# Kernel optimization log

Hardware: AMD Instinct MI355X
Metric: run time of the kernel (lower is better)

The kernel has to match this reference:

```python
import jax, jax.numpy as jnp
import numpy as np

N = 50000          # nodes
E = 400000         # edges (before self loops)
F_IN = 128         # NUM_FEATURES
HID = 32           # hidden_dim
H = 12             # heads
HC = H * HID       # concat dim = 384
CLASSES = 40       # NUM_CLASSES
NEG_SLOPE = 0.2    # PyG GATv2 default


def setup_inputs() -> dict:
    key = jax.random.key(0)
    ks = jax.random.split(key, 16)

    def p(k, shape, fan_in):
        return (jax.random.normal(k, shape, jnp.float32) / np.sqrt(fan_in)).astype(jnp.float32)

    return {
        "x": jax.random.normal(ks[0], (N, F_IN), jnp.float32),
        "edge_index": jax.random.randint(ks[1], (2, E), 0, N, jnp.int32),
        # GATv2 layer 1 (share_weights=False)
        "Wl1": p(ks[2], (F_IN, HC), F_IN),
        "Wr1": p(ks[3], (F_IN, HC), F_IN),
        "a1": p(ks[4], (H, HID), HID),
        "b1": jnp.zeros((HC,), jnp.float32),
        # GATv2 layer 2
        "Wl2": p(ks[5], (HC, HC), HC),
        "Wr2": p(ks[6], (HC, HC), HC),
        "a2": p(ks[7], (H, HID), HID),
        "b2": jnp.zeros((HC,), jnp.float32),
        # MLP head
        "W3": p(ks[8], (HC, HID), HC),
        "b3": jnp.zeros((HID,), jnp.float32),
        "W4": p(ks[9], (HID, CLASSES), HID),
        "b4": jnp.zeros((CLASSES,), jnp.float32),
    }


def _gatv2(x, Wl, Wr, att, bias, src, dst):
    # source/target linear projections, per-head
    xl = (x @ Wl).reshape(-1, H, HID)   # [N,H,C] (message features)
    xr = (x @ Wr).reshape(-1, H, HID)   # [N,H,C]
    # per-edge attention logits: a^T LeakyReLU(xl_src + xr_dst)
    e = jax.nn.leaky_relu(xl[src] + xr[dst], NEG_SLOPE)   # [E',H,C]
    logit = jnp.einsum('ehc,hc->eh', e, att)              # [E',H]
    # segment softmax over incoming edges per dst node (self loops guarantee nonempty)
    m = jax.ops.segment_max(logit, dst, num_segments=N)   # [N,H]
    ex = jnp.exp(logit - m[dst])
    denom = jax.ops.segment_sum(ex, dst, num_segments=N)  # [N,H]
    alpha = ex / denom[dst]                                # [E',H]
    # weighted scatter-add of source messages
    out = jax.ops.segment_sum(xl[src] * alpha[:, :, None], dst, num_segments=N)
    return out.reshape(-1, HC) + bias


def reference(x, edge_index, Wl1, Wr1, a1, b1, Wl2, Wr2, a2, b2, W3, b3, W4, b4):
    # add_self_loops=True (PyG default)
    loops = jnp.arange(N, dtype=edge_index.dtype)
    src = jnp.concatenate([edge_index[0], loops])
    dst = jnp.concatenate([edge_index[1], loops])
    # dropout p=0.6 is identity in eval mode
    h = _gatv2(x, Wl1, Wr1, a1, b1, src, dst)
    h = jax.nn.elu(h)
    h = _gatv2(h, Wl2, Wr2, a2, b2, src, dst)
    h = jax.nn.elu(h)
    h = jax.nn.elu(h @ W3 + b3)
    h = h @ W4 + b4
    return jax.nn.log_softmax(h, axis=1)
```

## Files before the change

kernel.cpp:

```cpp
#include <hip/hip_runtime.h>
#include <hip/hip_bf16.h>
#include <math.h>

#define N_NODES 50000
#define E_EDGES 400000
#define EN_TOT  (E_EDGES + N_NODES)
#define F_IN    128
#define HC      384
#define CLASSES 40
#define LOG2E   1.44269504088896f

typedef short short8 __attribute__((ext_vector_type(8)));
typedef float floatx4 __attribute__((ext_vector_type(4)));
typedef float floatx2 __attribute__((ext_vector_type(2)));
typedef unsigned int uint;

struct u3 { uint x, y, z; };

__device__ __forceinline__ float bf2f(unsigned short u) {
  union { unsigned int i; float f; } x; x.i = ((unsigned int)u) << 16; return x.f;
}
__device__ __forceinline__ unsigned short f2bf(float f) {
  union { float f; unsigned int i; } x; x.f = f;
  unsigned int r = x.i + 0x7fffu + ((x.i >> 16) & 1u);
  return (unsigned short)(r >> 16);
}
__device__ __forceinline__ float fin(float v) {
  return (fabsf(v) < 1e30f) ? v : 0.f;
}
__device__ __forceinline__ float rdw(const void* p, int idx, int fp32) {
  return fp32 ? ((const float*)p)[idx] : bf2f(((const unsigned short*)p)[idx]);
}

#if __has_builtin(__builtin_amdgcn_exp2f)
#define EXP2F(x) __builtin_amdgcn_exp2f(x)
#else
#define EXP2F(x) exp2f(x)
#endif

#if __has_builtin(__builtin_amdgcn_update_dpp)
#define DPP_ADD(w, ctrl) \
  (w += __int_as_float(__builtin_amdgcn_update_dpp(0, __float_as_int(w), ctrl, 0xf, 0xf, true)))
#define REDUCE16(w) do { DPP_ADD(w, 0xB1); DPP_ADD(w, 0x4E); DPP_ADD(w, 0x141); DPP_ADD(w, 0x140); } while (0)
#define DPP_MAXF(w, ctrl) do { float _t = __int_as_float(__builtin_amdgcn_update_dpp(0, \
    __float_as_int(w), ctrl, 0xf, 0xf, true)); w = fmaxf(w, _t); } while (0)
#define RED16MAX(w) do { DPP_MAXF(w, 0xB1); DPP_MAXF(w, 0x4E); DPP_MAXF(w, 0x141); DPP_MAXF(w, 0x140); } while (0)
#else
#define REDUCE16(w) do { w += __shfl_xor(w, 1); w += __shfl_xor(w, 2); \
                         w += __shfl_xor(w, 4); w += __shfl_xor(w, 8); } while (0)
#define RED16MAX(w) do { w = fmaxf(w, __shfl_xor(w, 1)); w = fmaxf(w, __shfl_xor(w, 2)); \
                         w = fmaxf(w, __shfl_xor(w, 4)); w = fmaxf(w, __shfl_xor(w, 8)); } while (0)
#endif


__global__ void k_sentinel(float* out, int n) {
  int i = blockIdx.x * 256 + threadIdx.x;
  if (i < n) out[i] = 111.0f;
}

__global__ void k_detect_zero(const unsigned short* __restrict__ x, int* __restrict__ flag,
                              int* __restrict__ counts, int* __restrict__ cursor) {
  int i = blockIdx.x * 256 + threadIdx.x;
  if (i < N_NODES) { counts[i] = 0; cursor[i] = 0; }
  if (blockIdx.x == 0 && threadIdx.x < 64) {
    int L = threadIdx.x;
    int sane = 0;
#pragma unroll
    for (int t = 0; t < 4; ++t) {
      unsigned short u = x[(size_t)(L * 4 + t) * 2];
      unsigned int mag = u & 0x7FFFu;
      unsigned int e   = (u >> 7) & 0xFFu;
      if (mag == 0u || (e >= 96u && e <= 159u)) sane++;
    }
    sane += __shfl_xor(sane, 1);
    sane += __shfl_xor(sane, 2);
    sane += __shfl_xor(sane, 4);
    sane += __shfl_xor(sane, 8);
    sane += __shfl_xor(sane, 16);
    sane += __shfl_xor(sane, 32);
    if (L == 0) flag[0] = (sane < 179) ? 1 : 0;
  }
}

__global__ void k_cvt(const void* __restrict__ x, unsigned short* __restrict__ Xb,
                      const int* __restrict__ flagp) {
  int i = blockIdx.x * 256 + threadIdx.x;
  if (i >= N_NODES * F_IN / 8) return;
  if (flagp[0]) {
    const floatx4* p = (const floatx4*)x + (size_t)i * 2;
    floatx4 f0 = p[0], f1 = p[1];
    short8 o;
#pragma unroll
    for (int j = 0; j < 4; ++j) { o[j] = (short)f2bf(f0[j]); o[4 + j] = (short)f2bf(f1[j]); }
    ((short8*)Xb)[i] = o;
  } else {
    ((short8*)Xb)[i] = ((const short8*)x)[i];
  }
}

__global__ void k_count(const int* __restrict__ ei, int* __restrict__ counts) {
  int e = blockIdx.x * 256 + threadIdx.x;
  if (e >= EN_TOT) return;
  int dst = (e < E_EDGES) ? ei[E_EDGES + e] : (e - E_EDGES);
  if ((unsigned)dst < N_NODES) atomicAdd(&counts[dst], 1);
}

__global__ void k_scan1(const int* __restrict__ counts, int* __restrict__ row_start,
                        int* __restrict__ bsum) {
  int b = blockIdx.x, tid = threadIdx.x;
  int i = b * 1024 + tid;
  int v = (i < N_NODES) ? counts[i] : 0;
  int lane = tid & 63, w = tid >> 6;
  int x = v;
#pragma unroll
  for (int d = 1; d < 64; d <<= 1) { int t = __shfl_up(x, d); if (lane >= d) x += t; }
  __shared__ int wsum[16];
  if (lane == 63) wsum[w] = x;
  __syncthreads();
  if (w == 0) {
    int y = (lane < 16) ? wsum[lane] : 0;
#pragma unroll
    for (int d = 1; d < 16; d <<= 1) { int t = __shfl_up(y, d); if (lane >= d) y += t; }
    if (lane < 16) wsum[lane] = y;
  }
  __syncthreads();
  if (w > 0) x += wsum[w - 1];
  if (i < N_NODES) row_start[i + 1] = x;
  if (tid == 1023) bsum[b] = x;
}

__global__ void k_scan23(int* __restrict__ row_start, const int* __restrict__ bsum, int nb) {
  int b = blockIdx.x, tid = threadIdx.x;
  __shared__ int sadd;
  if (tid < 64) {
    int lane = tid;
    int x = (lane < nb) ? bsum[lane] : 0;
#pragma unroll
    for (int d = 1; d < 64; d <<= 1) { int t = __shfl_up(x, d); if (lane >= d) x += t; }
    int pre = __shfl(x, (b > 0) ? (b - 1) : 0);
    if (tid == 0) sadd = (b > 0) ? pre : 0;
  }
  __syncthreads();
  int add = sadd;
  int i = b * 1024 + tid;
  if (i < N_NODES) row_start[i + 1] += add;
  if (i == 0) row_start[0] = 0;
}

__global__ void k_fill(const int* __restrict__ ei, const int* __restrict__ row_start,
                       int* __restrict__ cursor, int* __restrict__ csr_off) {
  int e = blockIdx.x * 256 + threadIdx.x;
  if (e >= EN_TOT) return;
  int src, dst;
  if (e < E_EDGES) { src = ei[e]; dst = ei[E_EDGES + e]; }
  else             { src = dst = e - E_EDGES; }
  if ((unsigned)dst >= N_NODES) return;
  int sv = ((unsigned)src < N_NODES) ? src : 0;
  int pos = atomicAdd(&cursor[dst], 1);
  int slot = row_start[dst] + pos;
  if ((unsigned)slot < EN_TOT) csr_off[slot] = sv * 768;
}

#define PK_J1 (F_IN * HC)
#define PK_J2 (2 * PK_J1)
#define PK_J3 (PK_J2 + HC * HC)
#define PK_J4 (PK_J3 + HC * HC)
#define PK_J5 (PK_J4 + HC * 32)
#define PK_J6 (PK_J5 + 32 * 48)
#define PK_EX 3144
#define PK_TOT (PK_J6 + PK_EX)
__global__ void k_pack_all(const void* __restrict__ Wl1, const void* __restrict__ Wr1,
                           const void* __restrict__ Wl2, const void* __restrict__ Wr2,
                           const void* __restrict__ W3, const void* __restrict__ W4,
                           const void* __restrict__ a1_, const void* __restrict__ a2_,
                           const void* __restrict__ b1_, const void* __restrict__ b2_,
                           const void* __restrict__ b3_, const void* __restrict__ b4_,
                           unsigned short* __restrict__ BpL1, unsigned short* __restrict__ BpR1,
                           unsigned short* __restrict__ BpL2, unsigned short* __restrict__ BpR2,
                           unsigned short* __restrict__ Bp3, unsigned short* __restrict__ Bp4,
                           float* __restrict__ attp1, float* __restrict__ attp2,
                           float* __restrict__ biasp1, float* __restrict__ biasp2,
                           float* __restrict__ b3p, float* __restrict__ b4p,
                           const int* __restrict__ flagp) {
  int gid = blockIdx.x * 256 + threadIdx.x;
  if (gid >= PK_TOT) return;
  int fp32 = flagp[0];
  if (gid >= PK_J6) {
    int i = gid - PK_J6;
    if (i < 3072) {
      int seg = i / 768, r = i % 768;
      int L = r / 6, q = r % 6, k = q >> 1, b = q & 1;
      int c = 2 * L + 128 * k + b;
      if (seg == 0)      attp1[r]  = fin(rdw(a1_, c, fp32)) * LOG2E;
      else if (seg == 1) attp2[r]  = fin(rdw(a2_, c, fp32)) * LOG2E;
      else if (seg == 2) biasp1[r] = fin(rdw(b1_, c, fp32));
      else               biasp2[r] = fin(rdw(b2_, c, fp32));
    } else if (i < 3104) b3p[i - 3072] = fin(rdw(b3_, i - 3072, fp32));
    else                 b4p[i - 3104] = fin(rdw(b4_, i - 3104, fp32));
    return;
  }
  const void* src; unsigned short* dst; int NT, NCOL, idx;
  if (gid < PK_J2)      { NT = 24; NCOL = 384; if (gid < PK_J1) { src = Wl1; dst = BpL1; idx = gid; }
                                               else             { src = Wr1; dst = BpR1; idx = gid - PK_J1; } }
  else if (gid < PK_J4) { NT = 24; NCOL = 384; if (gid < PK_J3) { src = Wl2; dst = BpL2; idx = gid - PK_J2; }
                                               else             { src = Wr2; dst = BpR2; idx = gid - PK_J3; } }
  else if (gid < PK_J5) { NT = 2;  NCOL = 32;  src = W3; dst = Bp3; idx = gid - PK_J4; }
  else                  { NT = 3;  NCOL = 40;  src = W4; dst = Bp4; idx = gid - PK_J5; }
  int j  = idx & 7;
  int L  = (idx >> 3) & 63;
  int t  = idx >> 9;
  int nt = t % NT;
  int kt = t / NT;
  int k  = kt * 32 + ((L >> 4) * 8) + j;
  int n  = nt * 16 + (L & 15);
  float v = (n < NCOL) ? rdw(src, k * NCOL + n, fp32) : 0.f;
  dst[idx] = f2bf(fin(v));
}

#define LOADB(dst, kt) do { _Pragma("unroll") for (int n = 0; n < 6; ++n) \
    dst[n] = ((const short8*)Bp)[((size_t)((kt) * 24 + nt0 + n)) * 64 + lane]; } while (0)
#define DOMFMA(bf, kt) do { \
    short8 af[2]; \
    _Pragma("unroll") for (int mf = 0; mf < 2; ++mf) { \
      int row = mf * 16 + rsel; \
      int col = (kt) * 64 + kk16 * 16; \
      af[mf] = *(const short8*)(smem + row * RS + (col ^ ((row & 7) << 4))); } \
    _Pragma("unroll") for (int n = 0; n < 6; ++n) \
      _Pragma("unroll") for (int mf = 0; mf < 2; ++mf) \
        acc[mf][n] = __builtin_amdgcn_mfma_f32_16x16x32_bf16(af[mf], bf[n], acc[mf][n], 0, 0, 0); } while (0)

template<int NK>
__global__ __launch_bounds__(256, 4) void k_gemm2(const unsigned short* __restrict__ A_,
                       const unsigned short* __restrict__ BpL,
                       const unsigned short* __restrict__ BpR,
                       unsigned short* __restrict__ CL, unsigned short* __restrict__ CR) {
  constexpr int RS  = NK * 64;
  constexpr int NST = NK / 2;
  __shared__ __align__(16) char smem[32 * 776];
  int which = blockIdx.x & 1;
  int bt    = blockIdx.x >> 1;
  const unsigned short* Bp = which ? BpR : BpL;
  unsigned short* C        = which ? CR  : CL;
  int tid  = threadIdx.x;
  int wave = tid >> 6, lane = tid & 63;
  int m0   = bt * 32;

  {
    uint4 v[NST];
#pragma unroll
    for (int i = 0; i < NST; ++i) {
      int o   = (i * 256 + tid) * 16;
      int row = o / RS;
      int rem = o - row * RS;
      int rg  = m0 + row; if (rg >= N_NODES) rg = N_NODES - 1;
      v[i] = *(const uint4*)((const char*)A_ + (size_t)rg * RS + rem);
    }
#pragma unroll
    for (int i = 0; i < NST; ++i) {
      int o   = (i * 256 + tid) * 16;
      int row = o / RS;
      int rem = o - row * RS;
      *(uint4*)(smem + row * RS + (rem ^ ((row & 7) << 4))) = v[i];
    }
  }

  int nt0  = wave * 6;
  int kk16 = (lane >> 4);
  int rsel = lane & 15;
  floatx4 acc[2][6];
#pragma unroll
  for (int mf = 0; mf < 2; ++mf)
#pragma unroll
    for (int n = 0; n < 6; ++n) acc[mf][n] = (floatx4){0.f, 0.f, 0.f, 0.f};

  short8 b0[6], b1[6], b2[6];
  LOADB(b0, 0);
  LOADB(b1, 1);
  __syncthreads();

#pragma unroll
  for (int kt = 0; kt < NK; ++kt) {
    if (kt + 2 < NK) {
      if (((kt + 2) % 3) == 0)      LOADB(b0, kt + 2);
      else if (((kt + 2) % 3) == 1) LOADB(b1, kt + 2);
      else                          LOADB(b2, kt + 2);
    }
    if ((kt % 3) == 0)      DOMFMA(b0, kt);
    else if ((kt % 3) == 1) DOMFMA(b1, kt);
    else                    DOMFMA(b2, kt);
  }

  __syncthreads();
  int qr = lane >> 4, ccol = lane & 15;
#pragma unroll
  for (int n = 0; n < 6; ++n) {
    int c    = (nt0 + n) * 16 + ccol;
    int soff = ((c & 127) >> 1) * 12 + (c >> 7) * 4 + (c & 1) * 2;
#pragma unroll
    for (int mf = 0; mf < 2; ++mf)
#pragma unroll
      for (int r = 0; r < 4; ++r) {
        int row = mf * 16 + qr * 4 + r;
        *(unsigned short*)(smem + row * 776 + soff) = f2bf(fin(acc[mf][n][r]));
      }
  }
  __syncthreads();
#pragma unroll
  for (int j = 0; j < 8; ++j) {
    int row = wave * 8 + j;
    int rg  = m0 + row;
    if (rg < N_NODES) {
      u3 val = *(const u3*)(smem + row * 776 + lane * 12);
      *(u3*)((char*)C + (size_t)rg * 768 + lane * 12) = val;
    }
  }
}

#define EBODY(q) do { \
    uint _qa[3] = {(q).x, (q).y, (q).z}; \
    _Pragma("unroll") \
    for (int k = 0; k < 3; ++k) { \
      floatx2 sv; \
      sv.x = __uint_as_float(_qa[k] << 16); \
      sv.y = __uint_as_float(_qa[k] & 0xffff0000u); \
      floatx2 t = sv + r2[k]; \
      t = __builtin_elementwise_max(t, t * 0.2f); \
      floatx2 dw = t * a2[k]; \
      float w = dw.x + dw.y; \
      REDUCE16(w); \
      w = fminf(fmaxf(w, -126.f), 126.f); \
      float p = EXP2F(w); \
      l[k] += p; \
      floatx2 pv = {p, p}; \
      acc[k] += pv * sv; \
    } } while (0)

__global__ void k_edge(const unsigned short* __restrict__ XL, const unsigned short* __restrict__ XR,
                       const int* __restrict__ row_start, const int* __restrict__ csr_off,
                       const float* __restrict__ attp, const float* __restrict__ biasp,
                       unsigned short* __restrict__ H) {
  int v = blockIdx.x;
  int L = threadIdx.x;
  int Lo = L * 12;
  floatx2 r2[3], a2[3];
  u3 rv3 = *(const u3*)((const char*)XR + (size_t)v * 768 + Lo);
  uint rr[3] = {rv3.x, rv3.y, rv3.z};
  const floatx2* ap = (const floatx2*)(attp + L * 6);
#pragma unroll
  for (int k = 0; k < 3; ++k) {
    r2[k].x = __uint_as_float(rr[k] << 16);
    r2[k].y = __uint_as_float(rr[k] & 0xffff0000u);
    a2[k] = ap[k];
  }
  float l[3] = {0.f, 0.f, 0.f};
  floatx2 acc[3];
#pragma unroll
  for (int k = 0; k < 3; ++k) acc[k] = (floatx2){0.f, 0.f};
  int beg = row_start[v], end = row_start[v + 1];
  if (beg < 0) beg = 0;
  if (end > EN_TOT) end = EN_TOT;
  const char* XLb = (const char*)XL;
  const unsigned OMAX = (N_NODES - 1) * 768u;
  for (int base = beg; base < end; base += 64) {
    int nE = end - base; if (nE > 64) nE = 64;
    int last = nE - 1;
    int offv = (base + L < end) ? csr_off[base + L] : 0;
#define RLD(i) ({ int _i = (i) > last ? last : (i); \
                  int _s = __builtin_amdgcn_readlane(offv, _i); \
                  if ((unsigned)_s > OMAX) _s = 0; \
                  *(const u3*)(XLb + (unsigned)_s + Lo); })
    u3 q0 = RLD(0), q1 = RLD(1), q2 = RLD(2), q3 = RLD(3);
    int j = 0;
    for (; j + 4 <= nE; j += 4) {
      u3 n0 = RLD(j + 4), n1 = RLD(j + 5), n2 = RLD(j + 6), n3 = RLD(j + 7);
      EBODY(q0); EBODY(q1); EBODY(q2); EBODY(q3);
      q0 = n0; q1 = n1; q2 = n2; q3 = n3;
    }
    if (j < nE)     EBODY(q0);
    if (j + 1 < nE) EBODY(q1);
    if (j + 2 < nE) EBODY(q2);
#undef RLD
  }
  const floatx2* bp = (const floatx2*)(biasp + L * 6);
  uint* hr = (uint*)(H + (size_t)v * HC);
#pragma unroll
  for (int k = 0; k < 3; ++k) {
    floatx2 bb = bp[k];
    float inv = 1.f / fmaxf(l[k], 1e-30f);
    float o0 = acc[k].x * inv + bb.x;
    float o1 = acc[k].y * inv + bb.y;
    o0 = o0 > 0.f ? o0 : EXP2F(o0 * LOG2E) - 1.f;
    o1 = o1 > 0.f ? o1 : EXP2F(o1 * LOG2E) - 1.f;
    hr[L + 64 * k] = (uint)f2bf(fin(o0)) | ((uint)f2bf(fin(o1)) << 16);
  }
}

__global__ void k_mlp(const unsigned short* __restrict__ H2,
                      const unsigned short* __restrict__ Bp3,
                      const unsigned short* __restrict__ Bp4,
                      const float* __restrict__ b3p, const float* __restrict__ b4p,
                      float* __restrict__ out) {
  __shared__ float hs[16][33];
  int lane = threadIdx.x;
  int m0   = blockIdx.x * 16;
  int row  = m0 + (lane & 15);
  int kk   = (lane >> 4) * 8;
  floatx4 acc[2];
  acc[0] = (floatx4){0.f, 0.f, 0.f, 0.f};
  acc[1] = (floatx4){0.f, 0.f, 0.f, 0.f};
#pragma unroll
  for (int kt = 0; kt < 12; ++kt) {
    short8 af = *(const short8*)(H2 + (size_t)row * HC + kt * 32 + kk);
    const short8* bp = (const short8*)Bp3 + (size_t)kt * 2 * 64 + lane;
    acc[0] = __builtin_amdgcn_mfma_f32_16x16x32_bf16(af, bp[0],  acc[0], 0, 0, 0);
    acc[1] = __builtin_amdgcn_mfma_f32_16x16x32_bf16(af, bp[64], acc[1], 0, 0, 0);
  }
  int qr = lane >> 4, cc = lane & 15;
#pragma unroll
  for (int nt = 0; nt < 2; ++nt)
#pragma unroll
    for (int r = 0; r < 4; ++r) {
      int col = nt * 16 + cc;
      float s = acc[nt][r] + b3p[col];
      s = s > 0.f ? s : EXP2F(s * LOG2E) - 1.f;
      hs[qr * 4 + r][col] = fin(s);
    }
  __syncthreads();
  short8 a2f;
#pragma unroll
  for (int j = 0; j < 8; ++j) a2f[j] = (short)f2bf(hs[lane & 15][kk + j]);
  floatx4 lg[3];
#pragma unroll
  for (int nt = 0; nt < 3; ++nt) {
    floatx4 z = (floatx4){0.f, 0.f, 0.f, 0.f};
    lg[nt] = __builtin_amdgcn_mfma_f32_16x16x32_bf16(a2f, ((const short8*)Bp4)[nt * 64 + lane], z, 0, 0, 0);
  }
  float bv[3];
#pragma unroll
  for (int nt = 0; nt < 3; ++nt) {
    int c = nt * 16 + cc;
    bv[nt] = (c < CLASSES) ? b4p[c] : 0.f;
  }
#pragma unroll
  for (int r = 0; r < 4; ++r) {
    float v0 = lg[0][r] + bv[0];
    float v1 = lg[1][r] + bv[1];
    float v2 = (cc < 8) ? (lg[2][r] + bv[2]) : -1e30f;
    float mx = fmaxf(fmaxf(v0, v1), v2);
    RED16MAX(mx);
    float sm = __expf(v0 - mx) + __expf(v1 - mx) + ((cc < 8) ? __expf(v2 - mx) : 0.f);
    sm = (sm == sm) ? sm : 1.f;
    REDUCE16(sm);
    float ls = mx + logf(sm);
    float* op = out + (size_t)(m0 + qr * 4 + r) * CLASSES;
    op[cc]      = fin(v0 - ls);
    op[16 + cc] = fin(v1 - ls);
    if (cc < 8) op[32 + cc] = fin(v2 - ls);
  }
}

extern "C" void kernel_launch(void* const* d_in, const int* in_sizes, int n_in,
                              void* d_out, int out_size, void* d_ws, size_t ws_size,
                              hipStream_t stream) {
  const void* x   = d_in[0];
  const int* ei   = (const int*)d_in[1];
  const void* Wl1 = d_in[2];
  const void* Wr1 = d_in[3];
  const void* a1  = d_in[4];
  const void* b1  = d_in[5];
  const void* Wl2 = d_in[6];
  const void* Wr2 = d_in[7];
  const void* a2  = d_in[8];
  const void* b2  = d_in[9];
  const void* W3  = d_in[10];
  const void* b3  = d_in[11];
  const void* W4  = d_in[12];
  const void* b4  = d_in[13];
  float* out = (float*)d_out;

  char* ws = (char*)d_ws;
  size_t off = 0;
  auto alloc = [&](size_t bytes) { size_t o = off; off += (bytes + 255) & ~(size_t)255; return o; };
  int* flag       = (int*)(ws + alloc(256));
  int* row_start  = (int*)(ws + alloc((size_t)(N_NODES + 1) * 4));
  int* counts     = (int*)(ws + alloc((size_t)N_NODES * 4));
  int* cursor     = (int*)(ws + alloc((size_t)N_NODES * 4));
  int* bsum       = (int*)(ws + alloc(64 * 4));
  int* csr_off    = (int*)(ws + alloc((size_t)EN_TOT * 4));
  unsigned short* BpL1 = (unsigned short*)(ws + alloc((size_t)F_IN * HC * 2));
  unsigned short* BpR1 = (unsigned short*)(ws + alloc((size_t)F_IN * HC * 2));
  unsigned short* BpL2 = (unsigned short*)(ws + alloc((size_t)HC * HC * 2));
  unsigned short* BpR2 = (unsigned short*)(ws + alloc((size_t)HC * HC * 2));
  unsigned short* Bp3  = (unsigned short*)(ws + alloc((size_t)HC * 32 * 2));
  unsigned short* Bp4  = (unsigned short*)(ws + alloc((size_t)32 * 48 * 2));
  float* attp1  = (float*)(ws + alloc(768 * 4));
  float* attp2  = (float*)(ws + alloc(768 * 4));
  float* biasp1 = (float*)(ws + alloc(768 * 4));
  float* biasp2 = (float*)(ws + alloc(768 * 4));
  float* b3p    = (float*)(ws + alloc(32 * 4));
  float* b4p    = (float*)(ws + alloc(40 * 4));
  unsigned short* Xb   = (unsigned short*)(ws + alloc((size_t)N_NODES * F_IN * 2));
  unsigned short* B0   = (unsigned short*)(ws + alloc((size_t)N_NODES * HC * 2));
  unsigned short* B1   = (unsigned short*)(ws + alloc((size_t)N_NODES * HC * 2));
  unsigned short* B2   = (unsigned short*)(ws + alloc((size_t)N_NODES * HC * 2));
  (void)in_sizes; (void)n_in;

  if (ws_size < off) {
    k_sentinel<<<(out_size + 255) / 256, 256, 0, stream>>>(out, out_size);
    return;
  }

  const int SCAN_BLOCKS = (N_NODES + 1023) / 1024;
  const int GEMM_BLOCKS = 2 * ((N_NODES + 31) / 32);
  const int CVT_BLOCKS  = (N_NODES * F_IN / 8 + 255) / 256;

  k_detect_zero<<<(N_NODES + 255) / 256, 256, 0, stream>>>((const unsigned short*)x, flag, counts, cursor);
  k_cvt<<<CVT_BLOCKS, 256, 0, stream>>>(x, Xb, flag);
  k_count<<<(EN_TOT + 255) / 256, 256, 0, stream>>>(ei, counts);
  k_scan1<<<SCAN_BLOCKS, 1024, 0, stream>>>(counts, row_start, bsum);
  k_scan23<<<SCAN_BLOCKS, 1024, 0, stream>>>(row_start, bsum, SCAN_BLOCKS);
  k_fill<<<(EN_TOT + 255) / 256, 256, 0, stream>>>(ei, row_start, cursor, csr_off);

  k_pack_all<<<(PK_TOT + 255) / 256, 256, 0, stream>>>(Wl1, Wr1, Wl2, Wr2, W3, W4,
                                                       a1, a2, b1, b2, b3, b4,
                                                       BpL1, BpR1, BpL2, BpR2, Bp3, Bp4,
                                                       attp1, attp2, biasp1, biasp2, b3p, b4p, flag);

  k_gemm2<4><<<GEMM_BLOCKS, 256, 0, stream>>>(Xb, BpL1, BpR1, B0, B1);
  k_edge<<<N_NODES, 64, 0, stream>>>(B0, B1, row_start, csr_off, attp1, biasp1, B1);

  k_gemm2<12><<<GEMM_BLOCKS, 256, 0, stream>>>(B1, BpL2, BpR2, B2, B0);
  k_edge<<<N_NODES, 64, 0, stream>>>(B2, B0, row_start, csr_off, attp2, biasp2, B1);

  k_mlp<<<N_NODES / 16, 64, 0, stream>>>(B1, Bp3, Bp4, b3p, b4p, out);
}
```

Measured before the change: 351.0 us.

## Fuse fp32-to-bf16 input conversion into first GEMM and deepen edge prefetch

Removes the standalone conversion kernel and its bf16 staging buffer: the first GEMM now reads fp32 x directly when the detect flag says so and converts while loading into shared memory. Zeroing of counts/cursor moves to a single memset on a merged buffer, and detection runs as a one-wave kernel. Separately, the edge aggregation loop now prefetches eight neighbour rows ahead instead of four, which raises memory-level parallelism at the cost of more registers. The GEMM's A load now reads twice as many bytes in fp32 mode, and both GEMM blocks (left and right) convert the same rows redundantly.

```diff
diff --git a/kernel.cpp b/kernel.cpp
--- a/kernel.cpp
+++ b/kernel.cpp
@@ -58,44 +58,23 @@
   if (i < n) out[i] = 111.0f;
 }
 
-__global__ void k_detect_zero(const unsigned short* __restrict__ x, int* __restrict__ flag,
-                              int* __restrict__ counts, int* __restrict__ cursor) {
-  int i = blockIdx.x * 256 + threadIdx.x;
-  if (i < N_NODES) { counts[i] = 0; cursor[i] = 0; }
-  if (blockIdx.x == 0 && threadIdx.x < 64) {
-    int L = threadIdx.x;
-    int sane = 0;
-#pragma unroll
-    for (int t = 0; t < 4; ++t) {
-      unsigned short u = x[(size_t)(L * 4 + t) * 2];
-      unsigned int mag = u & 0x7FFFu;
-      unsigned int e   = (u >> 7) & 0xFFu;
-      if (mag == 0u || (e >= 96u && e <= 159u)) sane++;
-    }
-    sane += __shfl_xor(sane, 1);
-    sane += __shfl_xor(sane, 2);
-    sane += __shfl_xor(sane, 4);
-    sane += __shfl_xor(sane, 8);
-    sane += __shfl_xor(sane, 16);
-    sane += __shfl_xor(sane, 32);
-    if (L == 0) flag[0] = (sane < 179) ? 1 : 0;
-  }
-}
-
-__global__ void k_cvt(const void* __restrict__ x, unsigned short* __restrict__ Xb,
-                      const int* __restrict__ flagp) {
-  int i = blockIdx.x * 256 + threadIdx.x;
-  if (i >= N_NODES * F_IN / 8) return;
-  if (flagp[0]) {
-    const floatx4* p = (const floatx4*)x + (size_t)i * 2;
-    floatx4 f0 = p[0], f1 = p[1];
-    short8 o;
-#pragma unroll
-    for (int j = 0; j < 4; ++j) { o[j] = (short)f2bf(f0[j]); o[4 + j] = (short)f2bf(f1[j]); }
-    ((short8*)Xb)[i] = o;
-  } else {
-    ((short8*)Xb)[i] = ((const short8*)x)[i];
-  }
+__global__ void k_detect(const unsigned short* __restrict__ x, int* __restrict__ flag) {
+  int L = threadIdx.x;
+  int sane = 0;
+#pragma unroll
+  for (int t = 0; t < 4; ++t) {
+    unsigned short u = x[(size_t)(L * 4 + t) * 2];
+    unsigned int mag = u & 0x7FFFu;
+    unsigned int e   = (u >> 7) & 0xFFu;
+    if (mag == 0u || (e >= 96u && e <= 159u)) sane++;
+  }
+  sane += __shfl_xor(sane, 1);
+  sane += __shfl_xor(sane, 2);
+  sane += __shfl_xor(sane, 4);
+  sane += __shfl_xor(sane, 8);
+  sane += __shfl_xor(sane, 16);
+  sane += __shfl_xor(sane, 32);
+  if (L == 0) flag[0] = (sane < 179) ? 1 : 0;
 }
 
 __global__ void k_count(const int* __restrict__ ei, int* __restrict__ counts) {
@@ -229,11 +208,12 @@
       _Pragma("unroll") for (int mf = 0; mf < 2; ++mf) \
         acc[mf][n] = __builtin_amdgcn_mfma_f32_16x16x32_bf16(af[mf], bf[n], acc[mf][n], 0, 0, 0); } while (0)
 
-template<int NK>
-__global__ __launch_bounds__(256, 4) void k_gemm2(const unsigned short* __restrict__ A_,
+template<int NK, int AF>
+__global__ __launch_bounds__(256, 4) void k_gemm2(const void* __restrict__ A_,
                        const unsigned short* __restrict__ BpL,
                        const unsigned short* __restrict__ BpR,
-                       unsigned short* __restrict__ CL, unsigned short* __restrict__ CR) {
+                       unsigned short* __restrict__ CL, unsigned short* __restrict__ CR,
+                       const int* __restrict__ flagp) {
   constexpr int RS  = NK * 64;
   constexpr int NST = NK / 2;
   __shared__ __align__(16) char smem[32 * 776];
@@ -241,6 +221,7 @@
   int bt    = blockIdx.x >> 1;
   const unsigned short* Bp = which ? BpR : BpL;
   unsigned short* C        = which ? CR  : CL;
+  int fp32 = AF ? flagp[0] : 0;
   int tid  = threadIdx.x;
   int wave = tid >> 6, lane = tid & 63;
   int m0   = bt * 32;
@@ -253,7 +234,17 @@
       int row = o / RS;
       int rem = o - row * RS;
       int rg  = m0 + row; if (rg >= N_NODES) rg = N_NODES - 1;
-      v[i] = *(const uint4*)((const char*)A_ + (size_t)rg * RS + rem);
+      if (AF && fp32) {
+        const float* p = (const float*)((const char*)A_ + ((size_t)rg * RS + rem) * 2);
+        floatx4 f0 = *(const floatx4*)p;
+        floatx4 f1 = *(const floatx4*)(p + 4);
+        short8 o8;
+#pragma unroll
+        for (int j = 0; j < 4; ++j) { o8[j] = (short)f2bf(f0[j]); o8[4 + j] = (short)f2bf(f1[j]); }
+        v[i] = *(uint4*)&o8;
+      } else {
+        v[i] = *(const uint4*)((const char*)A_ + (size_t)rg * RS + rem);
+      }
     }
 #pragma unroll
     for (int i = 0; i < NST; ++i) {
@@ -370,15 +361,23 @@
                   if ((unsigned)_s > OMAX) _s = 0; \
                   *(const u3*)(XLb + (unsigned)_s + Lo); })
     u3 q0 = RLD(0), q1 = RLD(1), q2 = RLD(2), q3 = RLD(3);
+    u3 q4 = RLD(4), q5 = RLD(5), q6 = RLD(6), q7 = RLD(7);
     int j = 0;
-    for (; j + 4 <= nE; j += 4) {
-      u3 n0 = RLD(j + 4), n1 = RLD(j + 5), n2 = RLD(j + 6), n3 = RLD(j + 7);
+    for (; j + 8 <= nE; j += 8) {
+      u3 n0 = RLD(j + 8),  n1 = RLD(j + 9),  n2 = RLD(j + 10), n3 = RLD(j + 11);
+      u3 n4 = RLD(j + 12), n5 = RLD(j + 13), n6 = RLD(j + 14), n7 = RLD(j + 15);
       EBODY(q0); EBODY(q1); EBODY(q2); EBODY(q3);
+      EBODY(q4); EBODY(q5); EBODY(q6); EBODY(q7);
       q0 = n0; q1 = n1; q2 = n2; q3 = n3;
+      q4 = n4; q5 = n5; q6 = n6; q7 = n7;
     }
     if (j < nE)     EBODY(q0);
     if (j + 1 < nE) EBODY(q1);
     if (j + 2 < nE) EBODY(q2);
+    if (j + 3 < nE) EBODY(q3);
+    if (j + 4 < nE) EBODY(q4);
+    if (j + 5 < nE) EBODY(q5);
+    if (j + 6 < nE) EBODY(q6);
 #undef RLD
   }
   const floatx2* bp = (const floatx2*)(biasp + L * 6);
@@ -483,8 +482,8 @@
   auto alloc = [&](size_t bytes) { size_t o = off; off += (bytes + 255) & ~(size_t)255; return o; };
   int* flag       = (int*)(ws + alloc(256));
   int* row_start  = (int*)(ws + alloc((size_t)(N_NODES + 1) * 4));
-  int* counts     = (int*)(ws + alloc((size_t)N_NODES * 4));
-  int* cursor     = (int*)(ws + alloc((size_t)N_NODES * 4));
+  int* counts     = (int*)(ws + alloc((size_t)2 * N_NODES * 4));
+  int* cursor     = counts + N_NODES;
   int* bsum       = (int*)(ws + alloc(64 * 4));
   int* csr_off    = (int*)(ws + alloc((size_t)EN_TOT * 4));
   unsigned short* BpL1 = (unsigned short*)(ws + alloc((size_t)F_IN * HC * 2));
@@ -499,7 +498,6 @@
   float* biasp2 = (float*)(ws + alloc(768 * 4));
   float* b3p    = (float*)(ws + alloc(32 * 4));
   float* b4p    = (float*)(ws + alloc(40 * 4));
-  unsigned short* Xb   = (unsigned short*)(ws + alloc((size_t)N_NODES * F_IN * 2));
   unsigned short* B0   = (unsigned short*)(ws + alloc((size_t)N_NODES * HC * 2));
   unsigned short* B1   = (unsigned short*)(ws + alloc((size_t)N_NODES * HC * 2));
   unsigned short* B2   = (unsigned short*)(ws + alloc((size_t)N_NODES * HC * 2));
@@ -512,10 +510,9 @@
 
   const int SCAN_BLOCKS = (N_NODES + 1023) / 1024;
   const int GEMM_BLOCKS = 2 * ((N_NODES + 31) / 32);
-  const int CVT_BLOCKS  = (N_NODES * F_IN / 8 + 255) / 256;
-
-  k_detect_zero<<<(N_NODES + 255) / 256, 256, 0, stream>>>((const unsigned short*)x, flag, counts, cursor);
-  k_cvt<<<CVT_BLOCKS, 256, 0, stream>>>(x, Xb, flag);
+
+  hipMemsetAsync(counts, 0, (size_t)2 * N_NODES * 4, stream);
+  k_detect<<<1, 64, 0, stream>>>((const unsigned short*)x, flag);
   k_count<<<(EN_TOT + 255) / 256, 256, 0, stream>>>(ei, counts);
   k_scan1<<<SCAN_BLOCKS, 1024, 0, stream>>>(counts, row_start, bsum);
   k_scan23<<<SCAN_BLOCKS, 1024, 0, stream>>>(row_start, bsum, SCAN_BLOCKS);
@@ -526,10 +523,10 @@
                                                        BpL1, BpR1, BpL2, BpR2, Bp3, Bp4,
                                                        attp1, attp2, biasp1, biasp2, b3p, b4p, flag);
 
-  k_gemm2<4><<<GEMM_BLOCKS, 256, 0, stream>>>(Xb, BpL1, BpR1, B0, B1);
+  k_gemm2<4, 1><<<GEMM_BLOCKS, 256, 0, stream>>>(x, BpL1, BpR1, B0, B1, flag);
   k_edge<<<N_NODES, 64, 0, stream>>>(B0, B1, row_start, csr_off, attp1, biasp1, B1);
 
-  k_gemm2<12><<<GEMM_BLOCKS, 256, 0, stream>>>(B1, BpL2, BpR2, B2, B0);
+  k_gemm2<12, 0><<<GEMM_BLOCKS, 256, 0, stream>>>(B1, BpL2, BpR2, B2, B0, flag);
   k_edge<<<N_NODES, 64, 0, stream>>>(B2, B0, row_start, csr_off, attp2, biasp2, B1);
 
   k_mlp<<<N_NODES / 16, 64, 0, stream>>>(B1, Bp3, Bp4, b3p, b4p, out);
```

New measurement: 366.6 us. +4.4%, slower.
